# Kernel optimization log

Measured on AMD Instinct MI355X. Metric: run time of the kernel, lower is better.

## Reference

```python
import jax, jax.numpy as jnp
import numpy as np

B, H, S, P = 4, 16, 1024, 64
D = H * P  # state_size = 1024


def setup_inputs() -> dict:
    key = jax.random.key(0)
    k0, k1, k2, k3, k4 = jax.random.split(key, 5)
    q = jax.random.normal(k0, (B * H, S, P), jnp.float32)
    k = jax.random.normal(k1, (B * H, S, P), jnp.float32)
    v = jax.random.normal(k2, (B * H, S, P), jnp.float32)
    # xavier_uniform for the merge projection (fan_in = fan_out = D)
    limit = np.sqrt(6.0 / (D + D)).astype(np.float32)
    w_merge = jax.random.uniform(k3, (D, D), jnp.float32, -limit, limit)
    # causal position mask: True = masked (as used by masked_fill)
    position_mask = jnp.triu(jnp.ones((S, S), dtype=bool), k=1)
    # source-length padding mask: True = padded position
    lengths = jax.random.randint(k4, (B,), S // 2, S + 1)
    src_length_mask = jnp.arange(S)[None, :] >= lengths[:, None]
    return {"q": q, "k": k, "v": v, "w_merge": w_merge,
            "position_mask": position_mask, "src_length_mask": src_length_mask}


def reference(q, k, v, w_merge, position_mask, src_length_mask):
    # q,k,v: [B*H, S, P]; position_mask: [S,S] bool; src_length_mask: [B,S] bool
    BH, T, Pp = q.shape
    nb = src_length_mask.shape[0]
    nh = BH // nb
    scale = 1.0 / np.sqrt(Pp).astype(np.float32)
    # logits = bmm(q, k^T) * scale
    logits = jnp.einsum('btp,bsp->bts', q, k) * scale  # [B*H, T, S]
    logits = logits.reshape(nb, nh, T, T)
    logits = jnp.where(position_mask[None, None, :, :], -jnp.inf, logits)
    logits = jnp.where(src_length_mask[:, None, None, :], -jnp.inf, logits)
    scores = jax.nn.softmax(logits, axis=-1).reshape(BH, T, T)
    # dropout is identity in eval / p=0
    data = jnp.einsum('bts,bsp->btp', scores, v)  # [B*H, T, P]
    # merge heads: [B, H, T, P] -> [B, T, H*P]
    data = data.reshape(nb, nh, T, Pp).transpose(0, 2, 1, 3).reshape(nb, T, nh * Pp)
    return data @ w_merge.T  # Linear(bias=False)
```

## Files before the change

### kernel.cpp

```cpp
#include <hip/hip_runtime.h>
#include <hip/hip_bf16.h>
#include <math.h>


typedef _Float16 f16x8 __attribute__((ext_vector_type(8)));
typedef unsigned short u16x8 __attribute__((ext_vector_type(8)));
typedef float f32x4 __attribute__((ext_vector_type(4)));

union H8 { u16x8 u; f16x8 h; };

static __device__ __forceinline__ unsigned short f2hu(float f) {
  _Float16 h = (_Float16)f;
  unsigned short u;
  __builtin_memcpy(&u, &h, 2);
  return u;
}

#define MFMA16(a, b, c) __builtin_amdgcn_mfma_f32_16x16x32_f16((a), (b), (c), 0, 0, 0)

static __device__ __forceinline__ void gload16(const void* g, void* l) {
  __builtin_amdgcn_global_load_lds(
      (const __attribute__((address_space(1))) unsigned int*)g,
      (__attribute__((address_space(3))) unsigned int*)l, 16, 0, 0);
}

__global__ __launch_bounds__(256) void prep_all(const float* __restrict__ w,
                                                const int* __restrict__ smask,
                                                const float* __restrict__ kin,
                                                const float* __restrict__ vin,
                                                unsigned short* __restrict__ w_sw,
                                                unsigned short* __restrict__ k_sw,
                                                unsigned short* __restrict__ v_sw,
                                                int* __restrict__ lengths) {
  const int bid = blockIdx.x;
  const int tid = threadIdx.x;
  if (bid < 4) {
    __shared__ int sh[256];
    int4 m = ((const int4*)(smask + bid * 1024))[tid];
    sh[tid] = (m.x != 0) + (m.y != 0) + (m.z != 0) + (m.w != 0);
    __syncthreads();
    for (int o = 128; o > 0; o >>= 1) {
      if (tid < o) sh[tid] += sh[tid + o];
      __syncthreads();
    }
    if (tid == 0) lengths[bid] = 1024 - sh[0];
  } else if (bid < 1028) {
    int idx = (bid - 4) * 256 + tid;
    float4 f = ((const float4*)w)[idx];
    ushort4 o;
    o.x = f2hu(f.x); o.y = f2hu(f.y); o.z = f2hu(f.z); o.w = f2hu(f.w);
    int row = idx >> 8;
    int c4 = (idx & 255) * 4;
    int nt = row >> 6, r = row & 63, kt = c4 >> 6, cb = (c4 & 63) * 2;
    *(ushort4*)((char*)w_sw + ((size_t)(nt * 16 + kt)) * 8192 +
                ((r * 128 + cb) ^ ((r & 7) << 4))) = o;
  } else if (bid < 3076) {
    int idx = (bid - 1028) * 256 + tid;
    const float4* src = ((const float4*)kin) + (size_t)idx * 2;
    float4 a = src[0], b = src[1];
    u16x8 o;
    o[0] = f2hu(a.x); o[1] = f2hu(a.y); o[2] = f2hu(a.z); o[3] = f2hu(a.w);
    o[4] = f2hu(b.x); o[5] = f2hu(b.y); o[6] = f2hu(b.z); o[7] = f2hu(b.w);
    int bh = idx >> 13;
    int i = idx & 8191;
    int s = i >> 3;
    int c16 = i & 7;
    int kt = s >> 6, r = s & 63;
    int xb = (r * 128 + c16 * 16) ^ ((r & 7) << 4);
    *(u16x8*)((char*)k_sw + ((size_t)(bh * 16 + kt)) * 8192 + xb) = o;
  } else {
    const int t = bid - 3076;
    const int bh = t >> 4;
    const int st = t & 15;
    __shared__ unsigned short T[64][72];
    const float* vp = vin + ((size_t)bh * 1024 + st * 64) * 64;
#pragma unroll
    for (int i = 0; i < 4; ++i) {
      int e = i * 256 + tid;
      int row = e >> 4;
      int c4 = (e & 15) * 4;
      float4 f = *(const float4*)(vp + row * 64 + c4);
      T[c4 + 0][row] = f2hu(f.x);
      T[c4 + 1][row] = f2hu(f.y);
      T[c4 + 2][row] = f2hu(f.z);
      T[c4 + 3][row] = f2hu(f.w);
    }
    __syncthreads();
#pragma unroll
    for (int i = 0; i < 4; ++i) {
      int e = i * 256 + tid;
      int feat = e >> 4;
      int c4 = (e & 15) * 4;
      ushort4 o;
      o.x = T[feat][c4 + 0]; o.y = T[feat][c4 + 1];
      o.z = T[feat][c4 + 2]; o.w = T[feat][c4 + 3];
      int xb = (feat * 128 + c4 * 2) ^ ((feat & 7) << 4);
      *(ushort4*)((char*)v_sw + ((size_t)(bh * 16 + st)) * 8192 + xb) = o;
    }
  }
}

static __device__ __forceinline__ void qset_step(const unsigned short* Kcur,
                                                 const unsigned short* Vcur,
                                                 char* Pw, const H8 qa[2],
                                                 f32x4 (&oacc)[4], f32x4& sumacc,
                                                 int kt, int qbase, int len,
                                                 int l15, int kgrp, int wv) {
  f32x4 sacc[4] = {};
  __builtin_amdgcn_s_setprio(1);
#pragma unroll
  for (int kb = 0; kb < 2; kb++)
#pragma unroll
    for (int nb = 0; nb < 4; nb++) {
      H8 bb;
      bb.u = *(const u16x8*)((const char*)Kcur +
              (((nb * 16 + l15) * 128 + (kb * 32 + kgrp * 8) * 2) ^ ((l15 & 7) << 4)));
      sacc[nb] = MFMA16(qa[kb].h, bb.h, sacc[nb]);
    }
  __builtin_amdgcn_s_setprio(0);

#pragma unroll
  for (int nb = 0; nb < 4; nb++) {
    int scol = kt * 64 + nb * 16 + l15;
#pragma unroll
    for (int r = 0; r < 4; r++) {
      int trow = qbase + wv * 16 + kgrp * 4 + r;
      float pv = (scol > trow || scol >= len)
                     ? 0.f
                     : __expf(fmaf(sacc[nb][r], 0.125f, -5.0f));
      int prow = kgrp * 4 + r;
      int pcol = nb * 16 + l15;
      *(unsigned short*)(Pw + ((prow * 128 + pcol * 2) ^ ((prow & 7) << 4))) = f2hu(pv);
    }
  }

  const f16x8 ones_h = {(_Float16)1.f, (_Float16)1.f, (_Float16)1.f, (_Float16)1.f,
                        (_Float16)1.f, (_Float16)1.f, (_Float16)1.f, (_Float16)1.f};
  __builtin_amdgcn_s_setprio(1);
#pragma unroll
  for (int kb = 0; kb < 2; kb++) {
    H8 pa;
    pa.u = *(const u16x8*)((const char*)Pw +
            ((l15 * 128 + (kb * 32 + kgrp * 8) * 2) ^ ((l15 & 7) << 4)));
    sumacc = MFMA16(pa.h, ones_h, sumacc);
#pragma unroll
    for (int nb = 0; nb < 4; nb++) {
      H8 vb;
      vb.u = *(const u16x8*)((const char*)Vcur +
              (((nb * 16 + l15) * 128 + (kb * 32 + kgrp * 8) * 2) ^ ((l15 & 7) << 4)));
      oacc[nb] = MFMA16(pa.h, vb.h, oacc[nb]);
    }
  }
  __builtin_amdgcn_s_setprio(0);
}

static __device__ __forceinline__ void store_attn_sw(unsigned short* attn_sw,
                                                     int b, int h, int trow,
                                                     int nb, int l15, float v) {
  int grow = b * 1024 + trow;
  int mt = grow >> 7, rr = grow & 127;
  int cb = (nb * 16 + l15) * 2;
  *(unsigned short*)((char*)attn_sw + ((size_t)(mt * 16 + h)) * 16384 +
                     ((rr * 128 + cb) ^ ((rr & 7) << 4))) = f2hu(v);
}

__global__ __launch_bounds__(256, 2) void attn_pair(const float* __restrict__ q,
                                                    const unsigned short* __restrict__ k_sw,
                                                    const unsigned short* __restrict__ v_sw,
                                                    const int* __restrict__ lengths,
                                                    unsigned short* __restrict__ attn_sw) {
  const int wg = blockIdx.x;
  const int idx = (wg & 7) * 64 + (wg >> 3);
  const int bh = idx >> 3;
  const int p = idx & 7;
  const int qtA = p;
  const int qtB = 15 - p;
  const int b = bh >> 4;
  const int h = bh & 15;
  const int tid = threadIdx.x;
  const int lane = tid & 63;
  const int wv = tid >> 6;
  const int l15 = lane & 15;
  const int kgrp = lane >> 4;
  const int qbaseA = qtA * 64;
  const int qbaseB = qtB * 64;
  const int len = lengths[b];

  __shared__ __align__(16) unsigned short Kb[3][4096];
  __shared__ __align__(16) unsigned short Vb[3][4096];
  __shared__ __align__(16) unsigned short Plds[4][2][1024];

  const char* kbase_sw = (const char*)k_sw + (size_t)bh * 16 * 8192;
  const char* vbase_sw = (const char*)v_sw + (size_t)bh * 16 * 8192;
  char* PwA = (char*)(&Plds[wv][0][0]);
  char* PwB = (char*)(&Plds[wv][1][0]);

  H8 qaA[2], qaB[2];
  {
    const float* qpA = q + ((size_t)bh * 1024 + qbaseA + wv * 16 + l15) * 64;
    const float* qpB = q + ((size_t)bh * 1024 + qbaseB + wv * 16 + l15) * 64;
#pragma unroll
    for (int kb = 0; kb < 2; kb++) {
      const float* a0 = qpA + kb * 32 + kgrp * 8;
      float4 f0 = *(const float4*)(a0);
      float4 f1 = *(const float4*)(a0 + 4);
      u16x8 u;
      u[0] = f2hu(f0.x); u[1] = f2hu(f0.y); u[2] = f2hu(f0.z); u[3] = f2hu(f0.w);
      u[4] = f2hu(f1.x); u[5] = f2hu(f1.y); u[6] = f2hu(f1.z); u[7] = f2hu(f1.w);
      qaA[kb].u = u;
      const float* b0 = qpB + kb * 32 + kgrp * 8;
      float4 g0 = *(const float4*)(b0);
      float4 g1 = *(const float4*)(b0 + 4);
      u16x8 vv;
      vv[0] = f2hu(g0.x); vv[1] = f2hu(g0.y); vv[2] = f2hu(g0.z); vv[3] = f2hu(g0.w);
      vv[4] = f2hu(g1.x); vv[5] = f2hu(g1.y); vv[6] = f2hu(g1.z); vv[7] = f2hu(g1.w);
      qaB[kb].u = vv;
    }
  }

  f32x4 oaccA[4] = {}, oaccB[4] = {};
  f32x4 sumA = {}, sumB = {};

  const int nktA = qtA + 1;
  const int capB = (len - 1 < qbaseB + 63) ? (len - 1) : (qbaseB + 63);
  const int nktB = (capB >> 6) + 1;

#define STAGE_T(t, buf)                                                      \
  do {                                                                       \
    const char* ks_ = kbase_sw + (size_t)(t) * 8192;                         \
    const char* vs_ = vbase_sw + (size_t)(t) * 8192;                         \
    _Pragma("unroll") for (int j = 0; j < 2; ++j) {                          \
      int ch = wv * 2 + j;                                                   \
      gload16(ks_ + ch * 1024 + lane * 16, (char*)Kb[buf] + ch * 1024);      \
      gload16(vs_ + ch * 1024 + lane * 16, (char*)Vb[buf] + ch * 1024);      \
    }                                                                        \
  } while (0)

  STAGE_T(0, 0);
  STAGE_T(1, 1);

  for (int kt = 0; kt < nktB; ++kt) {
    const int cur = kt % 3;
    if (kt + 1 < nktB) {
      asm volatile("s_waitcnt vmcnt(4)" ::: "memory");
    } else {
      asm volatile("s_waitcnt vmcnt(0)" ::: "memory");
    }
    __builtin_amdgcn_s_barrier();
    if (kt + 2 < nktB) {
      const int nbuf = (kt + 2) % 3;
      STAGE_T(kt + 2, nbuf);
    }

    qset_step(Kb[cur], Vb[cur], PwB, qaB, oaccB, sumB, kt, qbaseB, len, l15, kgrp, wv);
    if (kt < nktA)
      qset_step(Kb[cur], Vb[cur], PwA, qaA, oaccA, sumA, kt, qbaseA, len, l15, kgrp, wv);
  }
#undef STAGE_T

#pragma unroll
  for (int nb = 0; nb < 4; nb++)
#pragma unroll
    for (int r = 0; r < 4; r++) {
      int trowA = qbaseA + wv * 16 + kgrp * 4 + r;
      store_attn_sw(attn_sw, b, h, trowA, nb, l15, oaccA[nb][r] / sumA[r]);
      int trowB = qbaseB + wv * 16 + kgrp * 4 + r;
      store_attn_sw(attn_sw, b, h, trowB, nb, l15, oaccB[nb][r] / sumB[r]);
    }
}

__global__ __launch_bounds__(256, 2) void merge_sw(const unsigned short* __restrict__ a_sw,
                                                   const unsigned short* __restrict__ w_sw,
                                                   float* __restrict__ out) {
  const int mt = blockIdx.x;
  const int nt = blockIdx.y;
  const int tid = threadIdx.x;
  const int lane = tid & 63;
  const int wv = tid >> 6;
  const int l15 = lane & 15;
  const int kgrp = lane >> 4;
  const int wr = wv >> 1;
  const int wc = wv & 1;

  __shared__ __align__(16) unsigned short Ab[3][8192];
  __shared__ __align__(16) unsigned short Wb[3][4096];

  const char* abase = (const char*)a_sw + (size_t)mt * 16 * 16384;
  const char* wbase = (const char*)w_sw + (size_t)nt * 16 * 8192;

  f32x4 acc[4][2] = {};

#define MSTAGE(t, buf)                                                    \
  do {                                                                    \
    const char* as_ = abase + (size_t)(t) * 16384;                        \
    const char* ws_ = wbase + (size_t)(t) * 8192;                         \
    _Pragma("unroll") for (int j = 0; j < 4; ++j) {                       \
      int ch = wv * 4 + j;                                                \
      gload16(as_ + ch * 1024 + lane * 16, (char*)Ab[buf] + ch * 1024);   \
    }                                                                     \
    _Pragma("unroll") for (int j = 0; j < 2; ++j) {                       \
      int ch = wv * 2 + j;                                                \
      gload16(ws_ + ch * 1024 + lane * 16, (char*)Wb[buf] + ch * 1024);   \
    }                                                                     \
  } while (0)

  MSTAGE(0, 0);
  MSTAGE(1, 1);

  for (int t = 0; t < 16; ++t) {
    const int cur = t % 3;
    if (t + 1 < 16) {
      asm volatile("s_waitcnt vmcnt(6)" ::: "memory");
    } else {
      asm volatile("s_waitcnt vmcnt(0)" ::: "memory");
    }
    __builtin_amdgcn_s_barrier();
    if (t + 2 < 16) MSTAGE(t + 2, (t + 2) % 3);

    __builtin_amdgcn_s_setprio(1);
#pragma unroll
    for (int kb = 0; kb < 2; kb++) {
      H8 wf[2];
#pragma unroll
      for (int nb = 0; nb < 2; nb++) {
        int wrow = wc * 32 + nb * 16 + l15;
        wf[nb].u = *(const u16x8*)((const char*)Wb[cur] +
                    ((wrow * 128 + (kb * 32 + kgrp * 8) * 2) ^ ((wrow & 7) << 4)));
      }
#pragma unroll
      for (int mb = 0; mb < 4; mb++) {
        int arow = wr * 64 + mb * 16 + l15;
        H8 aa;
        aa.u = *(const u16x8*)((const char*)Ab[cur] +
                ((arow * 128 + (kb * 32 + kgrp * 8) * 2) ^ ((arow & 7) << 4)));
#pragma unroll
        for (int nb = 0; nb < 2; nb++)
          acc[mb][nb] = MFMA16(aa.h, wf[nb].h, acc[mb][nb]);
      }
    }
    __builtin_amdgcn_s_setprio(0);
  }
#undef MSTAGE

  const int m0 = mt * 128, n0 = nt * 64;
#pragma unroll
  for (int mb = 0; mb < 4; mb++)
#pragma unroll
    for (int nb = 0; nb < 2; nb++)
#pragma unroll
      for (int r = 0; r < 4; r++)
        out[(size_t)(m0 + wr * 64 + mb * 16 + kgrp * 4 + r) * 1024 +
            n0 + wc * 32 + nb * 16 + l15] = acc[mb][nb][r];
}

extern "C" void kernel_launch(void* const* d_in, const int* in_sizes, int n_in,
                              void* d_out, int out_size, void* d_ws, size_t ws_size,
                              hipStream_t stream) {
  const float* q = (const float*)d_in[0];
  const float* k = (const float*)d_in[1];
  const float* v = (const float*)d_in[2];
  const float* w = (const float*)d_in[3];
  const int* smask = (const int*)d_in[5];
  float* out = (float*)d_out;

  char* ws = (char*)d_ws;
  const size_t MB = 1024 * 1024;
  int* lengths = (int*)ws;
  unsigned short* w_sw = (unsigned short*)(ws + 256);
  unsigned short* attn_sw = (unsigned short*)(ws + 256 + 2 * MB);
  unsigned short* k_sw = (unsigned short*)(ws + 256 + 10 * MB);
  unsigned short* v_sw = (unsigned short*)(ws + 256 + 18 * MB);

  hipLaunchKernelGGL(prep_all, dim3(4100), dim3(256), 0, stream,
                     w, smask, k, v, w_sw, k_sw, v_sw, lengths);
  hipLaunchKernelGGL(attn_pair, dim3(512), dim3(256), 0, stream,
                     q, k_sw, v_sw, lengths, attn_sw);
  hipLaunchKernelGGL(merge_sw, dim3(32, 16), dim3(256), 0, stream, attn_sw, w_sw, out);
}
```

Baseline: 58.16 us.

## Rewrite attention with 32x32 MFMA, register-resident P via permlane swap

The attention kernel switches from 16x16x32 MFMA tiles to 32x32x16 MFMA and computes S transposed (K as A operand), so the softmax probabilities can be packed and rearranged in registers with v_permlane32_swap instead of round-tripping through LDS. Each wave now owns 32 query rows of one of the two paired q-tiles (split across waves) rather than every wave processing both tiles, and row sums are accumulated in scalar registers instead of via an MFMA against ones. This removes LDS writes and reads for P and the extra sum MFMA, at the cost of more divergent per-wave work (waves with the short tile idle while the long tile runs) and bpermute at the end.

```diff
diff --git a/kernel.cpp b/kernel.cpp
--- a/kernel.cpp
+++ b/kernel.cpp
@@ -6,8 +6,10 @@
 typedef _Float16 f16x8 __attribute__((ext_vector_type(8)));
 typedef unsigned short u16x8 __attribute__((ext_vector_type(8)));
 typedef float f32x4 __attribute__((ext_vector_type(4)));
+typedef float f32x16 __attribute__((ext_vector_type(16)));
 
 union H8 { u16x8 u; f16x8 h; };
+union PAF { unsigned int w[4]; f16x8 h; };
 
 static __device__ __forceinline__ unsigned short f2hu(float f) {
   _Float16 h = (_Float16)f;
@@ -16,7 +18,17 @@
   return u;
 }
 
+static __device__ __forceinline__ unsigned int pk2(float lo, float hi) {
+  auto t = __builtin_amdgcn_cvt_pkrtz(lo, hi);
+  unsigned int u;
+  __builtin_memcpy(&u, &t, 4);
+  return u;
+}
+
+#define PLSWAP(a, b) asm("v_permlane32_swap_b32 %0, %1" : "+v"(a), "+v"(b))
+
 #define MFMA16(a, b, c) __builtin_amdgcn_mfma_f32_16x16x32_f16((a), (b), (c), 0, 0, 0)
+#define MFMA32(a, b, c) __builtin_amdgcn_mfma_f32_32x32x16_f16((a), (b), (c), 0, 0, 0)
 
 static __device__ __forceinline__ void gload16(const void* g, void* l) {
   __builtin_amdgcn_global_load_lds(
@@ -100,130 +112,67 @@
   }
 }
 
-static __device__ __forceinline__ void qset_step(const unsigned short* Kcur,
-                                                 const unsigned short* Vcur,
-                                                 char* Pw, const H8 qa[2],
-                                                 f32x4 (&oacc)[4], f32x4& sumacc,
-                                                 int kt, int qbase, int len,
-                                                 int l15, int kgrp, int wv) {
-  f32x4 sacc[4] = {};
-  __builtin_amdgcn_s_setprio(1);
-#pragma unroll
-  for (int kb = 0; kb < 2; kb++)
-#pragma unroll
-    for (int nb = 0; nb < 4; nb++) {
-      H8 bb;
-      bb.u = *(const u16x8*)((const char*)Kcur +
-              (((nb * 16 + l15) * 128 + (kb * 32 + kgrp * 8) * 2) ^ ((l15 & 7) << 4)));
-      sacc[nb] = MFMA16(qa[kb].h, bb.h, sacc[nb]);
-    }
-  __builtin_amdgcn_s_setprio(0);
-
-#pragma unroll
-  for (int nb = 0; nb < 4; nb++) {
-    int scol = kt * 64 + nb * 16 + l15;
-#pragma unroll
-    for (int r = 0; r < 4; r++) {
-      int trow = qbase + wv * 16 + kgrp * 4 + r;
-      float pv = (scol > trow || scol >= len)
-                     ? 0.f
-                     : __expf(fmaf(sacc[nb][r], 0.125f, -5.0f));
-      int prow = kgrp * 4 + r;
-      int pcol = nb * 16 + l15;
-      *(unsigned short*)(Pw + ((prow * 128 + pcol * 2) ^ ((prow & 7) << 4))) = f2hu(pv);
-    }
-  }
-
-  const f16x8 ones_h = {(_Float16)1.f, (_Float16)1.f, (_Float16)1.f, (_Float16)1.f,
-                        (_Float16)1.f, (_Float16)1.f, (_Float16)1.f, (_Float16)1.f};
-  __builtin_amdgcn_s_setprio(1);
-#pragma unroll
-  for (int kb = 0; kb < 2; kb++) {
-    H8 pa;
-    pa.u = *(const u16x8*)((const char*)Pw +
-            ((l15 * 128 + (kb * 32 + kgrp * 8) * 2) ^ ((l15 & 7) << 4)));
-    sumacc = MFMA16(pa.h, ones_h, sumacc);
-#pragma unroll
-    for (int nb = 0; nb < 4; nb++) {
-      H8 vb;
-      vb.u = *(const u16x8*)((const char*)Vcur +
-              (((nb * 16 + l15) * 128 + (kb * 32 + kgrp * 8) * 2) ^ ((l15 & 7) << 4)));
-      oacc[nb] = MFMA16(pa.h, vb.h, oacc[nb]);
-    }
-  }
-  __builtin_amdgcn_s_setprio(0);
-}
-
 static __device__ __forceinline__ void store_attn_sw(unsigned short* attn_sw,
-                                                     int b, int h, int trow,
-                                                     int nb, int l15, float v) {
+                                                     int b, int hh, int trow,
+                                                     int feat, float v) {
   int grow = b * 1024 + trow;
   int mt = grow >> 7, rr = grow & 127;
-  int cb = (nb * 16 + l15) * 2;
-  *(unsigned short*)((char*)attn_sw + ((size_t)(mt * 16 + h)) * 16384 +
+  int cb = feat * 2;
+  *(unsigned short*)((char*)attn_sw + ((size_t)(mt * 16 + hh)) * 16384 +
                      ((rr * 128 + cb) ^ ((rr & 7) << 4))) = f2hu(v);
 }
 
-__global__ __launch_bounds__(256, 2) void attn_pair(const float* __restrict__ q,
-                                                    const unsigned short* __restrict__ k_sw,
-                                                    const unsigned short* __restrict__ v_sw,
-                                                    const int* __restrict__ lengths,
-                                                    unsigned short* __restrict__ attn_sw) {
+__global__ __launch_bounds__(256, 2) void attn_w32(const float* __restrict__ q,
+                                                   const unsigned short* __restrict__ k_sw,
+                                                   const unsigned short* __restrict__ v_sw,
+                                                   const int* __restrict__ lengths,
+                                                   unsigned short* __restrict__ attn_sw) {
   const int wg = blockIdx.x;
   const int idx = (wg & 7) * 64 + (wg >> 3);
   const int bh = idx >> 3;
   const int p = idx & 7;
-  const int qtA = p;
   const int qtB = 15 - p;
   const int b = bh >> 4;
-  const int h = bh & 15;
+  const int hh = bh & 15;
   const int tid = threadIdx.x;
   const int lane = tid & 63;
   const int wv = tid >> 6;
-  const int l15 = lane & 15;
-  const int kgrp = lane >> 4;
-  const int qbaseA = qtA * 64;
-  const int qbaseB = qtB * 64;
+  const int l31 = lane & 31;
+  const int h = lane >> 5;
   const int len = lengths[b];
+
+  const int selB = ((wv >> 1) ^ (wg & 1)) & 1;
+  const int qt = selB ? qtB : p;
+  const int qb = qt * 64 + (wv & 1) * 32;
+  const int trow = qb + l31;
+
+  const int lcap = (len - 1) >> 6;
+  const int mynkt = ((lcap < qt) ? lcap : qt) + 1;
+  const int nktB = ((lcap < qtB) ? lcap : qtB) + 1;
 
   __shared__ __align__(16) unsigned short Kb[3][4096];
   __shared__ __align__(16) unsigned short Vb[3][4096];
-  __shared__ __align__(16) unsigned short Plds[4][2][1024];
 
   const char* kbase_sw = (const char*)k_sw + (size_t)bh * 16 * 8192;
   const char* vbase_sw = (const char*)v_sw + (size_t)bh * 16 * 8192;
-  char* PwA = (char*)(&Plds[wv][0][0]);
-  char* PwB = (char*)(&Plds[wv][1][0]);
-
-  H8 qaA[2], qaB[2];
+
+  H8 qf[4];
   {
-    const float* qpA = q + ((size_t)bh * 1024 + qbaseA + wv * 16 + l15) * 64;
-    const float* qpB = q + ((size_t)bh * 1024 + qbaseB + wv * 16 + l15) * 64;
-#pragma unroll
-    for (int kb = 0; kb < 2; kb++) {
-      const float* a0 = qpA + kb * 32 + kgrp * 8;
-      float4 f0 = *(const float4*)(a0);
-      float4 f1 = *(const float4*)(a0 + 4);
+    const float* qp = q + ((size_t)bh * 1024 + qb + l31) * 64;
+#pragma unroll
+    for (int c = 0; c < 4; ++c) {
+      const float* p0 = qp + c * 16 + h * 8;
+      float4 f0 = *(const float4*)(p0);
+      float4 f1 = *(const float4*)(p0 + 4);
       u16x8 u;
       u[0] = f2hu(f0.x); u[1] = f2hu(f0.y); u[2] = f2hu(f0.z); u[3] = f2hu(f0.w);
       u[4] = f2hu(f1.x); u[5] = f2hu(f1.y); u[6] = f2hu(f1.z); u[7] = f2hu(f1.w);
-      qaA[kb].u = u;
-      const float* b0 = qpB + kb * 32 + kgrp * 8;
-      float4 g0 = *(const float4*)(b0);
-      float4 g1 = *(const float4*)(b0 + 4);
-      u16x8 vv;
-      vv[0] = f2hu(g0.x); vv[1] = f2hu(g0.y); vv[2] = f2hu(g0.z); vv[3] = f2hu(g0.w);
-      vv[4] = f2hu(g1.x); vv[5] = f2hu(g1.y); vv[6] = f2hu(g1.z); vv[7] = f2hu(g1.w);
-      qaB[kb].u = vv;
-    }
-  }
-
-  f32x4 oaccA[4] = {}, oaccB[4] = {};
-  f32x4 sumA = {}, sumB = {};
-
-  const int nktA = qtA + 1;
-  const int capB = (len - 1 < qbaseB + 63) ? (len - 1) : (qbaseB + 63);
-  const int nktB = (capB >> 6) + 1;
+      qf[c].u = u;
+    }
+  }
+
+  f32x16 oacc0 = {}, oacc1 = {};
+  float psum = 0.f;
 
 #define STAGE_T(t, buf)                                                      \
   do {                                                                       \
@@ -247,26 +196,86 @@
       asm volatile("s_waitcnt vmcnt(0)" ::: "memory");
     }
     __builtin_amdgcn_s_barrier();
-    if (kt + 2 < nktB) {
-      const int nbuf = (kt + 2) % 3;
-      STAGE_T(kt + 2, nbuf);
-    }
-
-    qset_step(Kb[cur], Vb[cur], PwB, qaB, oaccB, sumB, kt, qbaseB, len, l15, kgrp, wv);
-    if (kt < nktA)
-      qset_step(Kb[cur], Vb[cur], PwA, qaA, oaccA, sumA, kt, qbaseA, len, l15, kgrp, wv);
+    if (kt + 2 < nktB) STAGE_T(kt + 2, (kt + 2) % 3);
+
+    if (kt < mynkt) {
+      const char* Kc = (const char*)Kb[cur];
+      const char* Vc = (const char*)Vb[cur];
+
+      f32x16 sacc0 = {}, sacc1 = {};
+      __builtin_amdgcn_s_setprio(1);
+#pragma unroll
+      for (int c = 0; c < 4; ++c) {
+        const int cb = c * 32 + h * 16;
+        H8 kf0, kf1;
+        kf0.u = *(const u16x8*)(Kc + ((l31 * 128 + cb) ^ ((l31 & 7) << 4)));
+        const int r1 = 32 + l31;
+        kf1.u = *(const u16x8*)(Kc + ((r1 * 128 + cb) ^ ((r1 & 7) << 4)));
+        sacc0 = MFMA32(kf0.h, qf[c].h, sacc0);
+        sacc1 = MFMA32(kf1.h, qf[c].h, sacc1);
+      }
+      __builtin_amdgcn_s_setprio(0);
+
+      unsigned int paw[4][4];
+      float ps = 0.f;
+#pragma unroll
+      for (int kb2 = 0; kb2 < 2; ++kb2) {
+        float pv[16];
+#pragma unroll
+        for (int r = 0; r < 16; ++r) {
+          float sv = kb2 ? sacc1[r] : sacc0[r];
+          int srl = (r & 3) + 8 * (r >> 2) + 4 * h;
+          int scol = kt * 64 + kb2 * 32 + srl;
+          float e = __expf(fmaf(sv, 0.125f, -5.0f));
+          pv[r] = (scol > trow || scol >= len) ? 0.f : e;
+          ps += pv[r];
+        }
+        unsigned int X0 = pk2(pv[0], pv[1]), X1 = pk2(pv[2], pv[3]);
+        unsigned int Y0 = pk2(pv[4], pv[5]), Y1 = pk2(pv[6], pv[7]);
+        unsigned int Z0 = pk2(pv[8], pv[9]), Z1 = pk2(pv[10], pv[11]);
+        unsigned int W0 = pk2(pv[12], pv[13]), W1 = pk2(pv[14], pv[15]);
+        PLSWAP(X0, Y0);
+        PLSWAP(X1, Y1);
+        PLSWAP(Z0, W0);
+        PLSWAP(Z1, W1);
+        paw[kb2 * 2 + 0][0] = X0; paw[kb2 * 2 + 0][1] = X1;
+        paw[kb2 * 2 + 0][2] = Y0; paw[kb2 * 2 + 0][3] = Y1;
+        paw[kb2 * 2 + 1][0] = Z0; paw[kb2 * 2 + 1][1] = Z1;
+        paw[kb2 * 2 + 1][2] = W0; paw[kb2 * 2 + 1][3] = W1;
+      }
+      psum += ps;
+
+      __builtin_amdgcn_s_setprio(1);
+#pragma unroll
+      for (int c = 0; c < 4; ++c) {
+        PAF pa;
+        pa.w[0] = paw[c][0]; pa.w[1] = paw[c][1];
+        pa.w[2] = paw[c][2]; pa.w[3] = paw[c][3];
+        const int cb = c * 32 + h * 16;
+        H8 vf0, vf1;
+        vf0.u = *(const u16x8*)(Vc + ((l31 * 128 + cb) ^ ((l31 & 7) << 4)));
+        const int r1 = 32 + l31;
+        vf1.u = *(const u16x8*)(Vc + ((r1 * 128 + cb) ^ ((r1 & 7) << 4)));
+        oacc0 = MFMA32(pa.h, vf0.h, oacc0);
+        oacc1 = MFMA32(pa.h, vf1.h, oacc1);
+      }
+      __builtin_amdgcn_s_setprio(0);
+    }
   }
 #undef STAGE_T
 
-#pragma unroll
-  for (int nb = 0; nb < 4; nb++)
-#pragma unroll
-    for (int r = 0; r < 4; r++) {
-      int trowA = qbaseA + wv * 16 + kgrp * 4 + r;
-      store_attn_sw(attn_sw, b, h, trowA, nb, l15, oaccA[nb][r] / sumA[r]);
-      int trowB = qbaseB + wv * 16 + kgrp * 4 + r;
-      store_attn_sw(attn_sw, b, h, trowB, nb, l15, oaccB[nb][r] / sumB[r]);
-    }
+  float sa = psum, sb = psum;
+  PLSWAP(sa, sb);
+  float inv = 1.0f / (sa + sb);
+#pragma unroll
+  for (int r = 0; r < 16; ++r) {
+    int crow = (r & 3) + 8 * (r >> 2) + 4 * h;
+    float invr = __int_as_float(
+        __builtin_amdgcn_ds_bpermute(crow << 2, __float_as_int(inv)));
+    int tr = qb + crow;
+    store_attn_sw(attn_sw, b, hh, tr, l31, oacc0[r] * invr);
+    store_attn_sw(attn_sw, b, hh, tr, 32 + l31, oacc1[r] * invr);
+  }
 }
 
 __global__ __launch_bounds__(256, 2) void merge_sw(const unsigned short* __restrict__ a_sw,
@@ -373,7 +382,7 @@
 
   hipLaunchKernelGGL(prep_all, dim3(4100), dim3(256), 0, stream,
                      w, smask, k, v, w_sw, k_sw, v_sw, lengths);
-  hipLaunchKernelGGL(attn_pair, dim3(512), dim3(256), 0, stream,
+  hipLaunchKernelGGL(attn_w32, dim3(512), dim3(256), 0, stream,
                      q, k_sw, v_sw, lengths, attn_sw);
   hipLaunchKernelGGL(merge_sw, dim3(32, 16), dim3(256), 0, stream, attn_sw, w_sw, out);
 }
```

Measured after the change: 63.46 us. +9.1%, slower.
